# Kernel tuning notes

Measured on AMD Instinct MI355X. Metric: run time of the kernel, lower is better.

Reference implementation:

```python
import jax, jax.numpy as jnp
import numpy as np

MUL = 32            # multiplicity of 0e and 1o irreps
IN_DIM = MUL * 4    # 32 scalars + 32 vectors = 128
SH_DIM = 4          # 1x0e + 1x1o
N_EDGE_FEAT = 128
HIDDEN = 128
W_NUMEL = 4 * MUL * MUL  # 4 CG paths, uvw weights 32x1x32 each
EPS = 1e-5
INV_SQRT3 = 1.0 / np.sqrt(3.0)
PATH_NORM = 1.0 / np.sqrt(2.0 * MUL)  # 2 paths per output irrep, fan-in MUL


def _fc(edge_attr, W1, b1, W2, b2):
    h = jax.nn.relu(edge_attr @ W1 + b1)
    return h @ W2 + b2  # [E, W_NUMEL]


def _tensor_product(x, sh, w):
    # FullyConnectedTensorProduct for (32x0e+32x1o) x (1x0e+1x1o) -> (32x0e+32x1o)
    # CG (real w3j): 0x0->0: 1 ; 0x1->1, 1x0->1, 1x1->0: delta/sqrt(3)
    E = x.shape[0]
    x0 = x[:, :MUL]                      # [E,32]   scalars
    x1 = x[:, MUL:].reshape(E, MUL, 3)   # [E,32,3] vectors
    sh0 = sh[:, 0]                       # [E]
    sh1 = sh[:, 1:4]                     # [E,3]
    wA = w[:, 0 * MUL * MUL:1 * MUL * MUL].reshape(E, MUL, MUL)  # 0e x 0e -> 0e
    wB = w[:, 1 * MUL * MUL:2 * MUL * MUL].reshape(E, MUL, MUL)  # 0e x 1o -> 1o
    wC = w[:, 2 * MUL * MUL:3 * MUL * MUL].reshape(E, MUL, MUL)  # 1o x 0e -> 1o
    wD = w[:, 3 * MUL * MUL:4 * MUL * MUL].reshape(E, MUL, MUL)  # 1o x 1o -> 0e
    out0 = PATH_NORM * (
        jnp.einsum('eu,euw->ew', x0 * sh0[:, None], wA)
        + INV_SQRT3 * jnp.einsum('eui,ei,euw->ew', x1, sh1, wD))
    out1 = PATH_NORM * INV_SQRT3 * (
        jnp.einsum('eu,ei,euw->ewi', x0, sh1, wB)
        + jnp.einsum('eui,euw->ewi', x1 * sh0[:, None, None], wC))
    return jnp.concatenate([out0, out1.reshape(E, MUL * 3)], axis=-1)  # [E,128]


def _batch_norm(x, bn_weight, bn_bias):
    # e3nn-style equivariant BatchNorm (training stats): scalars get mean/var
    # normalization + affine; vectors get norm normalization + scale.
    N = x.shape[0]
    s = x[:, :MUL]                       # [N,32]
    v = x[:, MUL:].reshape(N, MUL, 3)    # [N,32,3]
    s = s - s.mean(axis=0)
    s = s * (jax.lax.rsqrt((s ** 2).mean(axis=0) + EPS) * bn_weight[:MUL]) + bn_bias
    v_norm = jax.lax.rsqrt((v ** 2).mean(axis=-1).mean(axis=0) + EPS)  # [32]
    v = v * (v_norm * bn_weight[MUL:])[None, :, None]
    return jnp.concatenate([s, v.reshape(N, MUL * 3)], axis=-1)


def _forward(node_attr, edge_index, edge_attr, edge_sh,
             W1, b1, W2, b2, bn_weight, bn_bias):
    edge_src, edge_dst = edge_index[0], edge_index[1]
    N = node_attr.shape[0]
    w = _fc(edge_attr, W1, b1, W2, b2)                     # [E, 4096]
    tp = _tensor_product(node_attr[edge_dst], edge_sh, w)  # [E, 128]
    # scatter mean over edge_src
    summed = jax.ops.segment_sum(tp, edge_src, num_segments=N)
    counts = jax.ops.segment_sum(jnp.ones((tp.shape[0],), tp.dtype), edge_src,
                                 num_segments=N)
    out = summed / jnp.maximum(counts, 1.0)[:, None]
    out = out + node_attr                                  # residual (same dim, pad=0)
    return _batch_norm(out, bn_weight, bn_bias)


def setup_inputs() -> dict:
    key = jax.random.key(0)
    ks = jax.random.split(key, 10)
    N, E = 10000, 60000
    node_attr = jax.random.normal(ks[0], (N, IN_DIM), jnp.float32)
    edge_index = jax.random.randint(ks[1], (2, E), 0, N)
    edge_attr = jax.random.normal(ks[2], (E, N_EDGE_FEAT), jnp.float32)
    edge_sh = jax.random.normal(ks[3], (E, SH_DIM), jnp.float32)
    W1 = jax.random.normal(ks[4], (N_EDGE_FEAT, HIDDEN), jnp.float32) / np.sqrt(N_EDGE_FEAT)
    b1 = jnp.zeros((HIDDEN,), jnp.float32)
    W2 = jax.random.normal(ks[5], (HIDDEN, W_NUMEL), jnp.float32) / np.sqrt(HIDDEN)
    b2 = jnp.zeros((W_NUMEL,), jnp.float32)
    bn_weight = jnp.ones((2 * MUL,), jnp.float32)
    bn_bias = jnp.zeros((MUL,), jnp.float32)
    return {"node_attr": node_attr, "edge_index": edge_index,
            "edge_attr": edge_attr, "edge_sh": edge_sh,
            "W1": W1, "b1": b1, "W2": W2, "b2": b2,
            "bn_weight": bn_weight, "bn_bias": bn_bias}


def reference(node_attr, edge_index, edge_attr, edge_sh,
              W1, b1, W2, b2, bn_weight, bn_bias):
    return _forward(node_attr, edge_index, edge_attr, edge_sh,
                    W1, b1, W2, b2, bn_weight, bn_bias)
```

## Files before the change

### kernel.cpp

```cpp
#include <hip/hip_runtime.h>
#include <math.h>

#define EPSV 1e-5f
#define IS3  0.57735026918962576f
#define PNRM 0.125f

typedef __attribute__((ext_vector_type(8)))  short  short8;
typedef __attribute__((ext_vector_type(16))) float  floatx16;

static __device__ inline unsigned short f2bf(float f) {
    unsigned int u = __float_as_uint(f);
    return (unsigned short)((u + 0x7fff + ((u >> 16) & 1)) >> 16);
}
static __device__ inline float bflo(unsigned int u) { return __uint_as_float(u << 16); }
static __device__ inline float bfhi(unsigned int u) { return __uint_as_float(u & 0xffff0000u); }

#define GLD16(gp, lp) __builtin_amdgcn_global_load_lds( \
    (const __attribute__((address_space(1))) unsigned int*)(gp), \
    (__attribute__((address_space(3))) unsigned int*)(lp), 16, 0, 0)

__global__ __launch_bounds__(256) void k0_tile(const float* __restrict__ W2,
                                               const float* __restrict__ W1,
                                               unsigned short* __restrict__ W2T,
                                               unsigned short* __restrict__ W1T,
                                               int* __restrict__ zbase, int zn) {
    const int bx = blockIdx.x, tid = threadIdx.x;
    if (bx >= 132) {
        int i = (bx - 132) * 256 + tid;
        if (i < zn) zbase[i] = 0;
        return;
    }
    __shared__ float tile[128 * 33];
    const float* src;
    unsigned short* dst;
    int nc, tb;
    if (bx < 128) { src = W2; dst = W2T; nc = 4096; tb = bx; }
    else          { src = W1; dst = W1T; nc = 128;  tb = bx - 128; }
    const int c0 = tb * 32;
#pragma unroll
    for (int r = 0; r < 16; ++r) {
        int lin = r * 256 + tid;
        int k = lin >> 5, c = lin & 31;
        tile[k * 33 + c] = src[(size_t)k * nc + c0 + c];
    }
    __syncthreads();
#pragma unroll
    for (int r = 0; r < 2; ++r) {
        int g = r * 256 + tid;
        int kc = g >> 5, c = g & 31;
        short8 v;
#pragma unroll
        for (int j = 0; j < 8; ++j)
            v[j] = (short)f2bf(tile[(kc * 8 + j) * 33 + c]);
        *(short8*)(dst + (size_t)tb * 4096 + kc * 256 + c * 8) = v;
    }
}

__global__ __launch_bounds__(256) void k1_fc(const float* __restrict__ ea,
                                             const unsigned short* __restrict__ W1T,
                                             const float* __restrict__ b1,
                                             const int* __restrict__ ei,
                                             unsigned short* __restrict__ hsw,
                                             int* __restrict__ deg, int E) {
    __shared__ __align__(16) unsigned short W1s[16384];
    __shared__ __align__(16) unsigned short bounce[4 * 1056];
    const int tid = threadIdx.x, lane = tid & 63, wv = tid >> 6;
    const int half = lane >> 5, col = lane & 31;
    const int e0 = blockIdx.x * 128;

    if (tid < 128) { int e = e0 + tid; if (e < E) atomicAdd(&deg[ei[e]], 1); }

#pragma unroll
    for (int q = 0; q < 8; ++q) {
        int chunk = wv * 8 + q;
        GLD16((const char*)W1T + chunk * 1024 + lane * 16, (char*)W1s + chunk * 1024);
    }

    int e = e0 + wv * 32 + col; if (e >= E) e = E - 1;
    short8 afr[8];
#pragma unroll
    for (int c = 0; c < 8; ++c) {
        const float4* p = (const float4*)(ea + (size_t)e * 128 + c * 16 + half * 8);
        float4 f0 = p[0], f1 = p[1];
        short8 v;
        v[0] = (short)f2bf(f0.x); v[1] = (short)f2bf(f0.y);
        v[2] = (short)f2bf(f0.z); v[3] = (short)f2bf(f0.w);
        v[4] = (short)f2bf(f1.x); v[5] = (short)f2bf(f1.y);
        v[6] = (short)f2bf(f1.z); v[7] = (short)f2bf(f1.w);
        afr[c] = v;
    }
    __syncthreads();

    unsigned short* myb = bounce + wv * 1056;
    const int gg = blockIdx.x * 4 + wv;
#pragma unroll
    for (int jt = 0; jt < 4; ++jt) {
        floatx16 d = {0,0,0,0,0,0,0,0,0,0,0,0,0,0,0,0};
#pragma unroll
        for (int c = 0; c < 8; ++c) {
            short8 bf = *(const short8*)((const char*)W1s + jt * 8192 + (2 * c + half) * 512 + col * 16);
            d = __builtin_amdgcn_mfma_f32_32x32x16_bf16(afr[c], bf, d, 0, 0, 0);
        }
        float b1v = b1[jt * 32 + col];
#pragma unroll
        for (int reg = 0; reg < 16; ++reg) {
            int r = (reg & 3) + 8 * (reg >> 2) + 4 * half;
            float v = d[reg] + b1v;
            v = v > 0.f ? v : 0.f;
            myb[(col >> 3) * 264 + r * 8 + (col & 7)] = f2bf(v);
        }
#pragma unroll
        for (int s = 0; s < 2; ++s) {
            short8 v = *(const short8*)&myb[(s * 2 + (lane >> 5)) * 264 + (lane & 31) * 8];
            *(short8*)(hsw + (size_t)gg * 4096 + jt * 1024 + s * 512 + lane * 8) = v;
        }
    }
}

__global__ __launch_bounds__(256, 2) void k2_mfma(const unsigned short* __restrict__ hsw,
                                                  const unsigned short* __restrict__ W2T,
                                                  const float* __restrict__ b2,
                                                  const float* __restrict__ na,
                                                  const int* __restrict__ ei,
                                                  const float* __restrict__ sh,
                                                  const int* __restrict__ rowptr,
                                                  int* __restrict__ cursor,
                                                  int* __restrict__ elist,
                                                  float* __restrict__ tp, int E) {
    __shared__ __align__(16) char smem[32768];
    unsigned short* Ctb = (unsigned short*)smem;
    float* red = (float*)smem;

    const int tid = threadIdx.x, lane = tid & 63, wv = tid >> 6;
    const int half = lane >> 5, col = lane & 31;
    const int ust = wv >> 1, esub = wv & 1;
    const int e0 = blockIdx.x * 64;

    if (tid < 64) {
        int e = e0 + tid;
        if (e < E) {
            int s = ei[e];
            int pos = rowptr[s] + atomicAdd(&cursor[s], 1);
            elist[pos] = e;
        }
    }

    for (int idx = tid; idx < 2048; idx += 256) {
        int el = idx & 63, u = idx >> 6;
        int e = e0 + el; int ec = e < E ? e : E - 1;
        int dn = ei[E + ec];
        const float* nar = na + (size_t)dn * 128;
        float x0  = nar[u];
        float x10 = nar[32 + u * 3], x11 = nar[33 + u * 3], x12 = nar[34 + u * 3];
        const float* shr = sh + (size_t)ec * 4;
        float s0 = shr[0], s1 = shr[1], s2 = shr[2], s3 = shr[3];
        int o = u * 64 + el;
        Ctb[0 * 2048 + o] = f2bf(PNRM * x0 * s0);
        Ctb[1 * 2048 + o] = f2bf(PNRM * IS3 * x0);
        Ctb[2 * 2048 + o] = f2bf(PNRM * IS3 * s0 * x10);
        Ctb[3 * 2048 + o] = f2bf(PNRM * IS3 * s0 * x11);
        Ctb[4 * 2048 + o] = f2bf(PNRM * IS3 * s0 * x12);
        Ctb[5 * 2048 + o] = f2bf(PNRM * IS3 * (x10 * s1 + x11 * s2 + x12 * s3));
    }

    const int gg = blockIdx.x * 2 + esub;
    short8 afr[8];
#pragma unroll
    for (int c = 0; c < 8; ++c)
        afr[c] = *(const short8*)(hsw + (size_t)gg * 4096 + (2 * c + half) * 256 + col * 8);

    __syncthreads();

    float acc0[16] = {}, accB[16] = {}, accC0[16] = {}, accC1[16] = {}, accC2[16] = {};
    const int elb0 = esub * 32 + half * 4;
    const unsigned short* bbase = W2T + half * 256 + col * 8;

#define LOADB(p, br, b2r) do {                                         \
        int _ct = 2 * (p) + ust;                                       \
        const unsigned short* _bp = bbase + (size_t)_ct * 4096;        \
        _Pragma("unroll")                                              \
        for (int _c = 0; _c < 8; ++_c)                                 \
            (br)[_c] = *(const short8*)(_bp + _c * 512);               \
        (b2r) = b2[_ct * 32 + col];                                    \
    } while (0)

#define COMPUTE(p, br, b2v) do {                                                              \
        const int _ct = 2 * (p) + ust;                                                        \
        const int _b = _ct >> 5, _u = _ct & 31;                                               \
        floatx16 d = {0,0,0,0,0,0,0,0,0,0,0,0,0,0,0,0};                                       \
        _Pragma("unroll")                                                                     \
        for (int _c = 0; _c < 8; ++_c)                                                        \
            d = __builtin_amdgcn_mfma_f32_32x32x16_bf16(afr[_c], (br)[_c], d, 0, 0, 0);       \
        if (_b == 0 || _b == 3) {                                                             \
            const unsigned short* tb = Ctb + (_b == 0 ? 0 : 5) * 2048;                        \
            _Pragma("unroll")                                                                 \
            for (int q = 0; q < 4; ++q) {                                                     \
                uint2 cv = *(const uint2*)&tb[_u * 64 + elb0 + q * 8];                        \
                acc0[q * 4 + 0] += bflo(cv.x) * (d[q * 4 + 0] + (b2v));                       \
                acc0[q * 4 + 1] += bfhi(cv.x) * (d[q * 4 + 1] + (b2v));                       \
                acc0[q * 4 + 2] += bflo(cv.y) * (d[q * 4 + 2] + (b2v));                       \
                acc0[q * 4 + 3] += bfhi(cv.y) * (d[q * 4 + 3] + (b2v));                       \
            }                                                                                 \
        } else if (_b == 1) {                                                                 \
            _Pragma("unroll")                                                                 \
            for (int q = 0; q < 4; ++q) {                                                     \
                uint2 cv = *(const uint2*)&Ctb[1 * 2048 + _u * 64 + elb0 + q * 8];            \
                accB[q * 4 + 0] += bflo(cv.x) * (d[q * 4 + 0] + (b2v));                       \
                accB[q * 4 + 1] += bfhi(cv.x) * (d[q * 4 + 1] + (b2v));                       \
                accB[q * 4 + 2] += bflo(cv.y) * (d[q * 4 + 2] + (b2v));                       \
                accB[q * 4 + 3] += bfhi(cv.y) * (d[q * 4 + 3] + (b2v));                       \
            }                                                                                 \
        } else {                                                                              \
            _Pragma("unroll")                                                                 \
            for (int q = 0; q < 4; ++q) {                                                     \
                uint2 cu0 = *(const uint2*)&Ctb[2 * 2048 + _u * 64 + elb0 + q * 8];           \
                uint2 cu1 = *(const uint2*)&Ctb[3 * 2048 + _u * 64 + elb0 + q * 8];           \
                uint2 cu2 = *(const uint2*)&Ctb[4 * 2048 + _u * 64 + elb0 + q * 8];           \
                float f0[4] = {bflo(cu0.x), bfhi(cu0.x), bflo(cu0.y), bfhi(cu0.y)};           \
                float f1[4] = {bflo(cu1.x), bfhi(cu1.x), bflo(cu1.y), bfhi(cu1.y)};           \
                float f2[4] = {bflo(cu2.x), bfhi(cu2.x), bflo(cu2.y), bfhi(cu2.y)};           \
                _Pragma("unroll")                                                             \
                for (int rr = 0; rr < 4; ++rr) {                                              \
                    float v = d[q * 4 + rr] + (b2v);                                          \
                    accC0[q * 4 + rr] += f0[rr] * v;                                          \
                    accC1[q * 4 + rr] += f1[rr] * v;                                          \
                    accC2[q * 4 + rr] += f2[rr] * v;                                          \
                }                                                                             \
            }                                                                                 \
        }                                                                                     \
    } while (0)

    short8 bA[8], bB[8], bC[8];
    float b2A, b2B, b2C;
    LOADB(0, bA, b2A); LOADB(1, bB, b2B); LOADB(2, bC, b2C);
    for (int p = 0; p < 60; p += 3) {
        COMPUTE(p,     bA, b2A); LOADB(p + 3, bA, b2A);
        COMPUTE(p + 1, bB, b2B); LOADB(p + 4, bB, b2B);
        COMPUTE(p + 2, bC, b2C); LOADB(p + 5, bC, b2C);
    }
    COMPUTE(60, bA, b2A); LOADB(63, bA, b2A);
    COMPUTE(61, bB, b2B);
    COMPUTE(62, bC, b2C);
    COMPUTE(63, bA, b2A);
#undef LOADB
#undef COMPUTE

    __syncthreads();
    if (ust == 1) {
#pragma unroll
        for (int q = 0; q < 4; ++q) {
#pragma unroll
            for (int rr = 0; rr < 4; ++rr) {
                int reg = q * 4 + rr;
                int el = esub * 32 + q * 8 + half * 4 + rr;
                int e = e0 + el; int ec = e < E ? e : E - 1;
                float4 sv = *(const float4*)(sh + (size_t)ec * 4);
                red[(((esub * 4 + 0) * 16 + reg) << 6) + lane] = acc0[reg];
                red[(((esub * 4 + 1) * 16 + reg) << 6) + lane] = sv.y * accB[reg] + accC0[reg];
                red[(((esub * 4 + 2) * 16 + reg) << 6) + lane] = sv.z * accB[reg] + accC1[reg];
                red[(((esub * 4 + 3) * 16 + reg) << 6) + lane] = sv.w * accB[reg] + accC2[reg];
            }
        }
    }
    __syncthreads();
    if (ust == 0) {
#pragma unroll
        for (int q = 0; q < 4; ++q) {
#pragma unroll
            for (int rr = 0; rr < 4; ++rr) {
                int reg = q * 4 + rr;
                int el = esub * 32 + q * 8 + half * 4 + rr;
                int e = e0 + el;
                if (e >= E) continue;
                float4 sv = *(const float4*)(sh + (size_t)e * 4);
                float a0 = acc0[reg] + red[(((esub * 4 + 0) * 16 + reg) << 6) + lane];
                float o0 = sv.y * accB[reg] + accC0[reg] + red[(((esub * 4 + 1) * 16 + reg) << 6) + lane];
                float o1 = sv.z * accB[reg] + accC1[reg] + red[(((esub * 4 + 2) * 16 + reg) << 6) + lane];
                float o2 = sv.w * accB[reg] + accC2[reg] + red[(((esub * 4 + 3) * 16 + reg) << 6) + lane];
                float* tpe = tp + (size_t)e * 128;
                tpe[col] = a0;
                tpe[32 + col * 3 + 0] = o0;
                tpe[32 + col * 3 + 1] = o1;
                tpe[32 + col * 3 + 2] = o2;
            }
        }
    }
}

__global__ __launch_bounds__(1024) void k_scan(const int* __restrict__ deg,
                                               int* __restrict__ rowptr, int N) {
    __shared__ int part[1024];
    const int tid = threadIdx.x;
    const int chunk = (N + 1023) / 1024;
    const int base = tid * chunk;
    int s = 0;
    for (int i = 0; i < chunk; ++i) {
        int n = base + i;
        if (n < N) s += deg[n];
    }
    part[tid] = s;
    __syncthreads();
    for (int off = 1; off < 1024; off <<= 1) {
        int t = 0;
        if (tid >= off) t = part[tid - off];
        __syncthreads();
        if (tid >= off) part[tid] += t;
        __syncthreads();
    }
    int prefix = (tid == 0) ? 0 : part[tid - 1];
    for (int i = 0; i < chunk; ++i) {
        int n = base + i;
        if (n < N) { rowptr[n] = prefix; prefix += deg[n]; }
    }
    if (tid == 0) rowptr[N] = part[1023];
}

__global__ __launch_bounds__(256) void k4_gather(const float* __restrict__ tp,
                                                 const int* __restrict__ rowptr,
                                                 const int* __restrict__ elist,
                                                 const float* __restrict__ na,
                                                 float* __restrict__ pre,
                                                 float* __restrict__ stats, int N) {
    __shared__ float bns[96];
    const int tid = threadIdx.x;
    if (tid < 96) bns[tid] = 0.f;
    __syncthreads();
    const int o = tid & 127, hf = tid >> 7;
    for (int n = blockIdx.x * 2 + hf; n < N; n += gridDim.x * 2) {
        int r0 = rowptr[n], r1 = rowptr[n + 1];
        float s = 0.f;
        for (int j = r0; j < r1; ++j)
            s += tp[(size_t)elist[j] * 128 + o];
        int dg = r1 - r0;
        float cf = (float)(dg > 0 ? dg : 1);
        float v = s / cf + na[(size_t)n * 128 + o];
        pre[(size_t)n * 128 + o] = v;
        if (o < 32) {
            atomicAdd(&bns[o], v);
            atomicAdd(&bns[32 + o], v * v);
        } else {
            atomicAdd(&bns[64 + (o - 32) / 3], v * v);
        }
    }
    __syncthreads();
    if (tid < 96) atomicAdd(&stats[tid], bns[tid]);
}

__global__ __launch_bounds__(256) void k5_bn(const float* __restrict__ pre,
                                             const float* __restrict__ stats,
                                             const float* __restrict__ bnw,
                                             const float* __restrict__ bnb,
                                             float* __restrict__ out, int N) {
    size_t idx = (size_t)blockIdx.x * 256 + threadIdx.x;
    if (idx >= (size_t)N * 128) return;
    int o = (int)(idx & 127);
    float v = pre[idx];
    float invN = 1.f / (float)N;
    if (o < 32) {
        float m   = stats[o] * invN;
        float var = stats[32 + o] * invN - m * m;
        out[idx] = (v - m) * rsqrtf(var + EPSV) * bnw[o] + bnb[o];
    } else {
        int j = (o - 32) / 3;
        float vn = rsqrtf(stats[64 + j] * invN * (1.f / 3.f) + EPSV);
        out[idx] = v * vn * bnw[32 + j];
    }
}

extern "C" void kernel_launch(void* const* d_in, const int* in_sizes, int n_in,
                              void* d_out, int out_size, void* d_ws, size_t ws_size,
                              hipStream_t stream) {
    const float* node_attr  = (const float*)d_in[0];
    const int*   edge_index = (const int*)d_in[1];
    const float* edge_attr  = (const float*)d_in[2];
    const float* edge_sh    = (const float*)d_in[3];
    const float* W1  = (const float*)d_in[4];
    const float* b1  = (const float*)d_in[5];
    const float* W2  = (const float*)d_in[6];
    const float* b2  = (const float*)d_in[7];
    const float* bnw = (const float*)d_in[8];
    const float* bnb = (const float*)d_in[9];

    const int N = in_sizes[0] / 128;
    const int E = in_sizes[1] / 2;
    const int ngroups = ((E + 127) / 128) * 4;

    float* tp     = (float*)d_ws;
    float* pre    = tp + (size_t)E * 128;
    float* stats  = pre + (size_t)N * 128;
    int*   deg    = (int*)(stats + 96);
    int*   cursor = deg + N;
    int*   rowptr = cursor + N;
    int*   elist  = rowptr + N + 1;
    char* pbase = (char*)(elist + E);
    pbase += (16 - ((size_t)pbase & 15)) & 15;
    unsigned short* hsw = (unsigned short*)pbase;
    unsigned short* W2T = hsw + (size_t)ngroups * 4096;
    unsigned short* W1T = W2T + (size_t)524288;

    const int zn = 96 + 2 * N;
    const int zblocks = (zn + 255) / 256;

    k0_tile<<<132 + zblocks, 256, 0, stream>>>(W2, W1, W2T, W1T, (int*)stats, zn);
    k1_fc<<<(E + 127) / 128, 256, 0, stream>>>(edge_attr, W1T, b1, edge_index, hsw, deg, E);
    k_scan<<<1, 1024, 0, stream>>>(deg, rowptr, N);
    k2_mfma<<<(E + 63) / 64, 256, 0, stream>>>(hsw, W2T, b2, node_attr, edge_index,
                                               edge_sh, rowptr, cursor, elist, tp, E);
    k4_gather<<<1024, 256, 0, stream>>>(tp, rowptr, elist, node_attr, pre, stats, N);
    size_t ntot = (size_t)N * 128;
    k5_bn<<<(int)((ntot + 255) / 256), 256, 0, stream>>>(pre, stats, bnw, bnb,
                                                         (float*)d_out, N);
}
```

Before: 260.0 us.

## Scatter tensor-product outputs with float atomics instead of CSR gather

The MFMA kernel now atomically adds each edge's 128-wide result directly into the per-node accumulation buffer. This replaces the path that wrote a full per-edge tensor to memory, built a CSR edge list with a scan kernel, and then gathered. It removes the scan kernel, the per-edge intermediate write and read, and the indirect gather loop. In exchange it adds contended float atomics on L2/HBM and makes the summation order nondeterministic. The workspace is now zeroed with a memset instead of extra blocks in the tile kernel.

```diff
diff --git a/kernel.cpp b/kernel.cpp
--- a/kernel.cpp
+++ b/kernel.cpp
@@ -22,14 +22,8 @@
 __global__ __launch_bounds__(256) void k0_tile(const float* __restrict__ W2,
                                                const float* __restrict__ W1,
                                                unsigned short* __restrict__ W2T,
-                                               unsigned short* __restrict__ W1T,
-                                               int* __restrict__ zbase, int zn) {
+                                               unsigned short* __restrict__ W1T) {
     const int bx = blockIdx.x, tid = threadIdx.x;
-    if (bx >= 132) {
-        int i = (bx - 132) * 256 + tid;
-        if (i < zn) zbase[i] = 0;
-        return;
-    }
     __shared__ float tile[128 * 33];
     const float* src;
     unsigned short* dst;
@@ -123,10 +117,7 @@
                                                   const float* __restrict__ na,
                                                   const int* __restrict__ ei,
                                                   const float* __restrict__ sh,
-                                                  const int* __restrict__ rowptr,
-                                                  int* __restrict__ cursor,
-                                                  int* __restrict__ elist,
-                                                  float* __restrict__ tp, int E) {
+                                                  float* __restrict__ pre, int E) {
     __shared__ __align__(16) char smem[32768];
     unsigned short* Ctb = (unsigned short*)smem;
     float* red = (float*)smem;
@@ -135,15 +126,6 @@
     const int half = lane >> 5, col = lane & 31;
     const int ust = wv >> 1, esub = wv & 1;
     const int e0 = blockIdx.x * 64;
-
-    if (tid < 64) {
-        int e = e0 + tid;
-        if (e < E) {
-            int s = ei[e];
-            int pos = rowptr[s] + atomicAdd(&cursor[s], 1);
-            elist[pos] = e;
-        }
-    }
 
     for (int idx = tid; idx < 2048; idx += 256) {
         int el = idx & 63, u = idx >> 6;
@@ -277,64 +259,34 @@
                 float o0 = sv.y * accB[reg] + accC0[reg] + red[(((esub * 4 + 1) * 16 + reg) << 6) + lane];
                 float o1 = sv.z * accB[reg] + accC1[reg] + red[(((esub * 4 + 2) * 16 + reg) << 6) + lane];
                 float o2 = sv.w * accB[reg] + accC2[reg] + red[(((esub * 4 + 3) * 16 + reg) << 6) + lane];
-                float* tpe = tp + (size_t)e * 128;
-                tpe[col] = a0;
-                tpe[32 + col * 3 + 0] = o0;
-                tpe[32 + col * 3 + 1] = o1;
-                tpe[32 + col * 3 + 2] = o2;
+                int s = ei[e];
+                float* pr = pre + (size_t)s * 128;
+                unsafeAtomicAdd(&pr[col], a0);
+                unsafeAtomicAdd(&pr[32 + col * 3 + 0], o0);
+                unsafeAtomicAdd(&pr[32 + col * 3 + 1], o1);
+                unsafeAtomicAdd(&pr[32 + col * 3 + 2], o2);
             }
         }
     }
 }
 
-__global__ __launch_bounds__(1024) void k_scan(const int* __restrict__ deg,
-                                               int* __restrict__ rowptr, int N) {
-    __shared__ int part[1024];
-    const int tid = threadIdx.x;
-    const int chunk = (N + 1023) / 1024;
-    const int base = tid * chunk;
-    int s = 0;
-    for (int i = 0; i < chunk; ++i) {
-        int n = base + i;
-        if (n < N) s += deg[n];
-    }
-    part[tid] = s;
-    __syncthreads();
-    for (int off = 1; off < 1024; off <<= 1) {
-        int t = 0;
-        if (tid >= off) t = part[tid - off];
-        __syncthreads();
-        if (tid >= off) part[tid] += t;
-        __syncthreads();
-    }
-    int prefix = (tid == 0) ? 0 : part[tid - 1];
-    for (int i = 0; i < chunk; ++i) {
-        int n = base + i;
-        if (n < N) { rowptr[n] = prefix; prefix += deg[n]; }
-    }
-    if (tid == 0) rowptr[N] = part[1023];
-}
-
-__global__ __launch_bounds__(256) void k4_gather(const float* __restrict__ tp,
-                                                 const int* __restrict__ rowptr,
-                                                 const int* __restrict__ elist,
+__global__ __launch_bounds__(256) void k4_finish(float* __restrict__ pre,
+                                                 const int* __restrict__ deg,
                                                  const float* __restrict__ na,
-                                                 float* __restrict__ pre,
                                                  float* __restrict__ stats, int N) {
     __shared__ float bns[96];
     const int tid = threadIdx.x;
     if (tid < 96) bns[tid] = 0.f;
     __syncthreads();
-    const int o = tid & 127, hf = tid >> 7;
-    for (int n = blockIdx.x * 2 + hf; n < N; n += gridDim.x * 2) {
-        int r0 = rowptr[n], r1 = rowptr[n + 1];
-        float s = 0.f;
-        for (int j = r0; j < r1; ++j)
-            s += tp[(size_t)elist[j] * 128 + o];
-        int dg = r1 - r0;
+    const size_t total = (size_t)N * 128;
+    for (size_t idx = (size_t)blockIdx.x * 256 + tid; idx < total;
+         idx += (size_t)gridDim.x * 256) {
+        int o = (int)(idx & 127);
+        int n = (int)(idx >> 7);
+        int dg = deg[n];
         float cf = (float)(dg > 0 ? dg : 1);
-        float v = s / cf + na[(size_t)n * 128 + o];
-        pre[(size_t)n * 128 + o] = v;
+        float v = pre[idx] / cf + na[idx];
+        pre[idx] = v;
         if (o < 32) {
             atomicAdd(&bns[o], v);
             atomicAdd(&bns[32 + o], v * v);
@@ -385,28 +337,22 @@
     const int E = in_sizes[1] / 2;
     const int ngroups = ((E + 127) / 128) * 4;
 
-    float* tp     = (float*)d_ws;
-    float* pre    = tp + (size_t)E * 128;
-    float* stats  = pre + (size_t)N * 128;
-    int*   deg    = (int*)(stats + 96);
-    int*   cursor = deg + N;
-    int*   rowptr = cursor + N;
-    int*   elist  = rowptr + N + 1;
-    char* pbase = (char*)(elist + E);
+    float* pre   = (float*)d_ws;
+    float* stats = pre + (size_t)N * 128;
+    int*   deg   = (int*)(stats + 96);
+    char* pbase = (char*)(deg + N);
     pbase += (16 - ((size_t)pbase & 15)) & 15;
     unsigned short* hsw = (unsigned short*)pbase;
     unsigned short* W2T = hsw + (size_t)ngroups * 4096;
     unsigned short* W1T = W2T + (size_t)524288;
 
-    const int zn = 96 + 2 * N;
-    const int zblocks = (zn + 255) / 256;
-
-    k0_tile<<<132 + zblocks, 256, 0, stream>>>(W2, W1, W2T, W1T, (int*)stats, zn);
+    hipMemsetAsync(pre, 0, ((size_t)N * 128 + 96 + (size_t)N) * sizeof(float), stream);
+
+    k0_tile<<<132, 256, 0, stream>>>(W2, W1, W2T, W1T);
     k1_fc<<<(E + 127) / 128, 256, 0, stream>>>(edge_attr, W1T, b1, edge_index, hsw, deg, E);
-    k_scan<<<1, 1024, 0, stream>>>(deg, rowptr, N);
     k2_mfma<<<(E + 63) / 64, 256, 0, stream>>>(hsw, W2T, b2, node_attr, edge_index,
-                                               edge_sh, rowptr, cursor, elist, tp, E);
-    k4_gather<<<1024, 256, 0, stream>>>(tp, rowptr, elist, node_attr, pre, stats, N);
+                                               edge_sh, pre, E);
+    k4_finish<<<1024, 256, 0, stream>>>(pre, deg, node_attr, stats, N);
     size_t ntot = (size_t)N * 128;
     k5_bn<<<(int)((ntot + 255) / 256), 256, 0, stream>>>(pre, stats, bnw, bnb,
                                                          (float*)d_out, N);
```

Measured after the change: 273.2 us. 1.05x slower.
